# Optimization experiments

Hardware: AMD Instinct MI355X
Metric: run time of the kernel (lower is better)

Reference implementation:

```python
import jax, jax.numpy as jnp
import numpy as np

IN_FEATURES = 4096
OUT_FEATURES = 4096
GROUPS = 1
QB = 2 ** (8 - 1) - 1  # 127, int8 absmax quant


def setup_inputs() -> dict:
    key = jax.random.key(0)
    k_x, k_w = jax.random.split(key)
    x = jax.random.normal(k_x, (8192, IN_FEATURES), dtype=jnp.float32)
    # kaiming_uniform_(a=sqrt(5)) -> uniform(-1/sqrt(in), 1/sqrt(in))
    bound = 1.0 / np.sqrt(IN_FEATURES)
    weight = jax.random.uniform(
        k_w, (OUT_FEATURES, IN_FEATURES), dtype=jnp.float32,
        minval=-bound, maxval=bound)
    return {"input": x, "weight": weight}


def reference(input, weight):
    # --- ternarize weight per group ---
    w = weight.reshape(GROUPS, -1)                       # [G, out*in/G]
    w = w - jnp.mean(w, axis=1, keepdims=True)
    w = jnp.sign(w)
    # beta: per-group scale (note denominator uses full element count, as in source)
    beta = jnp.sum(jnp.abs(w), axis=1, keepdims=True) / (w.shape[0] * w.shape[1])
    w = (w * beta).reshape(OUT_FEATURES, IN_FEATURES)    # [out, in]

    # --- absmax int8 quantize activations (quantized values used, not dequant) ---
    scale = QB / jnp.max(jnp.abs(input))
    quant = jnp.round(scale * input)                     # [tokens, in]

    # --- linear + rescale ---
    out = quant @ w.T                                    # [tokens, out]
    out = out / beta.reshape(-1, 1)                      # groups=1: scalar divide
    return out
```

## Files before the change

kernel.cpp:

```cpp
#include <hip/hip_runtime.h>
#include <hip/hip_bf16.h>

typedef __attribute__((ext_vector_type(4))) int int4v;

#define TOKENS 8192
#define IN_F   4096
#define OUT_F  4096


__global__ void k_init(unsigned* maxbits) { *maxbits = 0u; }

__global__ __launch_bounds__(256) void k_wsum(const float4* __restrict__ w,
                                              double* __restrict__ partials) {
  __shared__ double sm[256];
  double s = 0.0;
  const float4* p = w + (size_t)blockIdx.x * 4096;
  for (int i = threadIdx.x; i < 4096; i += 256) {
    float4 v = p[i];
    s += (double)v.x + (double)v.y + (double)v.z + (double)v.w;
  }
  sm[threadIdx.x] = s;
  __syncthreads();
  for (int off = 128; off > 0; off >>= 1) {
    if (threadIdx.x < off) sm[threadIdx.x] += sm[threadIdx.x + off];
    __syncthreads();
  }
  if (threadIdx.x == 0) partials[blockIdx.x] = sm[0];
}

__global__ __launch_bounds__(256) void k_xmax(const float4* __restrict__ x,
                                              unsigned* __restrict__ maxbits) {
  float m = 0.f;
  const size_t n = (size_t)TOKENS * IN_F / 4;
  for (size_t i = (size_t)blockIdx.x * 256 + threadIdx.x; i < n;
       i += (size_t)gridDim.x * 256) {
    float4 v = x[i];
    m = fmaxf(m, fmaxf(fmaxf(fabsf(v.x), fabsf(v.y)),
                       fmaxf(fabsf(v.z), fabsf(v.w))));
  }
  __shared__ float sm[256];
  sm[threadIdx.x] = m;
  __syncthreads();
  for (int off = 128; off > 0; off >>= 1) {
    if (threadIdx.x < off) sm[threadIdx.x] = fmaxf(sm[threadIdx.x], sm[threadIdx.x + off]);
    __syncthreads();
  }
  if (threadIdx.x == 0) atomicMax(maxbits, __float_as_uint(sm[0]));
}

__global__ __launch_bounds__(256) void k_finalize(double* __restrict__ hdr,
                                                  const double* __restrict__ partials,
                                                  const unsigned* __restrict__ maxbits) {
  __shared__ double sm[256];
  double s = partials[threadIdx.x] + partials[threadIdx.x + 256] +
             partials[threadIdx.x + 512] + partials[threadIdx.x + 768];
  sm[threadIdx.x] = s;
  __syncthreads();
  for (int off = 128; off > 0; off >>= 1) {
    if (threadIdx.x < off) sm[threadIdx.x] += sm[threadIdx.x + off];
    __syncthreads();
  }
  if (threadIdx.x == 0) {
    hdr[0] = sm[0] / (double)((size_t)OUT_F * IN_F);
    hdr[1] = 127.0 / (double)__uint_as_float(*maxbits);
  }
}

__global__ __launch_bounds__(256) void k_quant(const float4* __restrict__ x,
                                               int* __restrict__ q,
                                               const double* __restrict__ hdr) {
  const double s = hdr[1];
  size_t i = (size_t)blockIdx.x * 256 + threadIdx.x;
  float4 v = x[i];
  int a = (int)rint(s * (double)v.x);
  int b = (int)rint(s * (double)v.y);
  int c = (int)rint(s * (double)v.z);
  int d = (int)rint(s * (double)v.w);
  q[i] = (a & 255) | ((b & 255) << 8) | ((c & 255) << 16) | ((d & 255) << 24);
}

__global__ __launch_bounds__(256) void k_tern(const float4* __restrict__ w,
                                              int* __restrict__ sgn,
                                              const double* __restrict__ hdr) {
  const double m = hdr[0];
  size_t i = (size_t)blockIdx.x * 256 + threadIdx.x;
  float4 v = w[i];
  int a = ((double)v.x > m) - ((double)v.x < m);
  int b = ((double)v.y > m) - ((double)v.y < m);
  int c = ((double)v.z > m) - ((double)v.z < m);
  int d = ((double)v.w > m) - ((double)v.w < m);
  sgn[i] = (a & 255) | ((b & 255) << 8) | ((c & 255) << 16) | ((d & 255) << 24);
}

__global__ __launch_bounds__(256) void k_gemm(const signed char* __restrict__ q,
                                              const signed char* __restrict__ s,
                                              float* __restrict__ out) {
  __shared__ signed char sA[128 * 128];
  __shared__ signed char sB[128 * 128];
  const int tid  = threadIdx.x;
  const int lane = tid & 63;
  const int wid  = tid >> 6;
  const int wr   = wid >> 1, wc = wid & 1;
  const int l15  = lane & 15, l4 = lane >> 4;
  const int bn = blockIdx.x & 31;
  const int bm = blockIdx.x >> 5;
  const size_t row0 = (size_t)bm * 128;
  const size_t col0 = (size_t)bn * 128;

  int4v acc[4][4];
#pragma unroll
  for (int i = 0; i < 4; ++i)
#pragma unroll
    for (int j = 0; j < 4; ++j) acc[i][j] = int4v{0, 0, 0, 0};

  for (int kt = 0; kt < 32; ++kt) {
    const int k0 = kt * 128;
    __syncthreads();
#pragma unroll
    for (int i = 0; i < 4; ++i) {
      const int idx_base = i * 256 + wid * 64;
      const int idx  = idx_base + lane;
      const int row  = idx >> 3;
      const int slot = idx & 7;
      const int koff = ((slot ^ (row & 7)) << 4);
      const signed char* gA = q + (row0 + row) * IN_F + k0 + koff;
      const signed char* gB = s + (col0 + row) * IN_F + k0 + koff;
      __builtin_amdgcn_global_load_lds(
          (const __attribute__((address_space(1))) void*)gA,
          (__attribute__((address_space(3))) void*)(sA + idx_base * 16), 16, 0, 0);
      __builtin_amdgcn_global_load_lds(
          (const __attribute__((address_space(1))) void*)gB,
          (__attribute__((address_space(3))) void*)(sB + idx_base * 16), 16, 0, 0);
    }
    __syncthreads();
#pragma unroll
    for (int ks = 0; ks < 2; ++ks) {
      int4v a[4], b[4];
#pragma unroll
      for (int f = 0; f < 4; ++f) {
        const int rowA = wr * 64 + f * 16 + l15;
        const int koff = ks * 64 + l4 * 16;
        a[f] = *(const int4v*)(sA + rowA * 128 + (koff ^ ((rowA & 7) << 4)));
        const int rowB = wc * 64 + f * 16 + l15;
        b[f] = *(const int4v*)(sB + rowB * 128 + (koff ^ ((rowB & 7) << 4)));
      }
#pragma unroll
      for (int fm = 0; fm < 4; ++fm)
#pragma unroll
        for (int fn = 0; fn < 4; ++fn)
          acc[fm][fn] = __builtin_amdgcn_mfma_i32_16x16x64_i8(a[fm], b[fn], acc[fm][fn], 0, 0, 0);
    }
  }

#pragma unroll
  for (int fm = 0; fm < 4; ++fm)
#pragma unroll
    for (int fn = 0; fn < 4; ++fn)
#pragma unroll
      for (int r = 0; r < 4; ++r) {
        const size_t rg = row0 + wr * 64 + fm * 16 + l4 * 4 + r;
        const size_t cg = col0 + wc * 64 + fn * 16 + l15;
        out[rg * OUT_F + cg] = (float)acc[fm][fn][r];
      }
}

extern "C" void kernel_launch(void* const* d_in, const int* in_sizes, int n_in,
                              void* d_out, int out_size, void* d_ws, size_t ws_size,
                              hipStream_t stream) {
  const float* x = (const float*)d_in[0];
  const float* w = (const float*)d_in[1];
  float* out = (float*)d_out;

  char* ws = (char*)d_ws;
  double*   hdr      = (double*)ws;
  unsigned* maxbits  = (unsigned*)(ws + 16);
  double*   partials = (double*)(ws + 1024);
  signed char* qbuf  = (signed char*)(ws + 16384);
  signed char* sbuf  = (signed char*)(ws + 16384 + (size_t)TOKENS * IN_F);

  k_init<<<1, 1, 0, stream>>>(maxbits);
  k_wsum<<<1024, 256, 0, stream>>>((const float4*)w, partials);
  k_xmax<<<2048, 256, 0, stream>>>((const float4*)x, maxbits);
  k_finalize<<<1, 256, 0, stream>>>(hdr, partials, maxbits);
  k_quant<<<(TOKENS * IN_F / 4) / 256, 256, 0, stream>>>((const float4*)x, (int*)qbuf, hdr);
  k_tern<<<(OUT_F * IN_F / 4) / 256, 256, 0, stream>>>((const float4*)w, (int*)sbuf, hdr);
  k_gemm<<<(TOKENS / 128) * (OUT_F / 128), 256, 0, stream>>>(qbuf, sbuf, out);
}
```

Baseline: 259.7 us.

## Rewrite int8 GEMM with 256x256 tiles and 4-stage async LDS pipeline

Replaces the 128x128 single-buffered GEMM with a 256x256 tile, 512-thread block that keeps a 4-deep ring of 64-wide K tiles in LDS. Global-to-LDS loads for future tiles are issued between interleaved MFMA halves, with explicit waitcnt, barriers and setprio to overlap memory with compute. It also swizzles the block index for L2 locality and changes the LDS XOR swizzle. The aim is to hide load latency and raise data reuse per block. The cost is a large accumulator register footprint and 128KB of LDS, which may limit occupancy, plus hand-placed synchronization that could be fragile.

Result: faster. 251.6 us (-3.1%).

```diff
diff --git a/kernel.cpp b/kernel.cpp
--- a/kernel.cpp
+++ b/kernel.cpp
@@ -92,75 +92,116 @@
   sgn[i] = (a & 255) | ((b & 255) << 8) | ((c & 255) << 16) | ((d & 255) << 24);
 }
 
-__global__ __launch_bounds__(256) void k_gemm(const signed char* __restrict__ q,
-                                              const signed char* __restrict__ s,
-                                              float* __restrict__ out) {
-  __shared__ signed char sA[128 * 128];
-  __shared__ signed char sB[128 * 128];
+__device__ __forceinline__ void stage2(const signed char* __restrict__ gsrc,
+                                       size_t grow0, int ktile,
+                                       signed char* ldsbase, int tid, int wid) {
+#pragma unroll
+  for (int i = 0; i < 2; ++i) {
+    const int slot = i * 512 + tid;
+    const int r = slot >> 2;
+    const int sir = slot & 3;
+    const signed char* g = gsrc + (grow0 + (size_t)r) * IN_F +
+                           (size_t)ktile * 64 + ((sir ^ (r & 3)) << 4);
+    __builtin_amdgcn_global_load_lds(
+        (const __attribute__((address_space(1))) void*)g,
+        (__attribute__((address_space(3))) void*)(ldsbase + (i * 512 + wid * 64) * 16),
+        16, 0, 0);
+  }
+}
+
+__global__ __launch_bounds__(512, 2) void k_gemm(const signed char* __restrict__ q,
+                                                 const signed char* __restrict__ s,
+                                                 float* __restrict__ out) {
+  __shared__ signed char sA[4][256 * 64];
+  __shared__ signed char sB[4][256 * 64];
   const int tid  = threadIdx.x;
   const int lane = tid & 63;
   const int wid  = tid >> 6;
-  const int wr   = wid >> 1, wc = wid & 1;
+  const int wm   = wid >> 2;
+  const int wn   = wid & 3;
   const int l15  = lane & 15, l4 = lane >> 4;
-  const int bn = blockIdx.x & 31;
-  const int bm = blockIdx.x >> 5;
-  const size_t row0 = (size_t)bm * 128;
-  const size_t col0 = (size_t)bn * 128;
-
-  int4v acc[4][4];
-#pragma unroll
-  for (int i = 0; i < 4; ++i)
+
+  const int swz = (blockIdx.x & 7) * 64 + (blockIdx.x >> 3);
+  const int bm = swz >> 4;
+  const int bn = swz & 15;
+  const size_t row0 = (size_t)bm * 256;
+  const size_t col0 = (size_t)bn * 256;
+
+  const int lane_off = l15 * 64 + ((l4 ^ (l15 & 3)) << 4);
+
+  int4v acc[8][4];
+#pragma unroll
+  for (int i = 0; i < 8; ++i)
 #pragma unroll
     for (int j = 0; j < 4; ++j) acc[i][j] = int4v{0, 0, 0, 0};
 
-  for (int kt = 0; kt < 32; ++kt) {
-    const int k0 = kt * 128;
-    __syncthreads();
-#pragma unroll
-    for (int i = 0; i < 4; ++i) {
-      const int idx_base = i * 256 + wid * 64;
-      const int idx  = idx_base + lane;
-      const int row  = idx >> 3;
-      const int slot = idx & 7;
-      const int koff = ((slot ^ (row & 7)) << 4);
-      const signed char* gA = q + (row0 + row) * IN_F + k0 + koff;
-      const signed char* gB = s + (col0 + row) * IN_F + k0 + koff;
-      __builtin_amdgcn_global_load_lds(
-          (const __attribute__((address_space(1))) void*)gA,
-          (__attribute__((address_space(3))) void*)(sA + idx_base * 16), 16, 0, 0);
-      __builtin_amdgcn_global_load_lds(
-          (const __attribute__((address_space(1))) void*)gB,
-          (__attribute__((address_space(3))) void*)(sB + idx_base * 16), 16, 0, 0);
+#pragma unroll
+  for (int t = 0; t < 3; ++t) {
+    stage2(q, row0, t, sA[t], tid, wid);
+    stage2(s, col0, t, sB[t], tid, wid);
+  }
+  asm volatile("s_waitcnt vmcnt(8)" ::: "memory");
+  __builtin_amdgcn_sched_barrier(0);
+  __builtin_amdgcn_s_barrier();
+  __builtin_amdgcn_sched_barrier(0);
+
+  for (int kt = 0; kt < 64; ++kt) {
+    const int c = kt & 3;
+    const int pf   = (kt + 3) & 63;
+    const int pbuf = (kt + 3) & 3;
+    const signed char* bufA = sA[c];
+    const signed char* bufB = sB[c];
+
+    int4v a[8], b0, b1;
+#pragma unroll
+    for (int m = 0; m < 8; ++m)
+      a[m] = *(const int4v*)(bufA + (wm * 128 + m * 16) * 64 + lane_off);
+    b0 = *(const int4v*)(bufB + (wn * 64 + 0) * 64 + lane_off);
+    b1 = *(const int4v*)(bufB + (wn * 64 + 16) * 64 + lane_off);
+    stage2(q, row0, pf, sA[pbuf], tid, wid);
+    __builtin_amdgcn_sched_barrier(0);
+    __builtin_amdgcn_s_barrier();
+    asm volatile("s_waitcnt lgkmcnt(0)" ::: "memory");
+    __builtin_amdgcn_sched_barrier(0);
+    __builtin_amdgcn_s_setprio(1);
+#pragma unroll
+    for (int m = 0; m < 8; ++m) {
+      acc[m][0] = __builtin_amdgcn_mfma_i32_16x16x64_i8(a[m], b0, acc[m][0], 0, 0, 0);
+      acc[m][1] = __builtin_amdgcn_mfma_i32_16x16x64_i8(a[m], b1, acc[m][1], 0, 0, 0);
     }
-    __syncthreads();
-#pragma unroll
-    for (int ks = 0; ks < 2; ++ks) {
-      int4v a[4], b[4];
-#pragma unroll
-      for (int f = 0; f < 4; ++f) {
-        const int rowA = wr * 64 + f * 16 + l15;
-        const int koff = ks * 64 + l4 * 16;
-        a[f] = *(const int4v*)(sA + rowA * 128 + (koff ^ ((rowA & 7) << 4)));
-        const int rowB = wc * 64 + f * 16 + l15;
-        b[f] = *(const int4v*)(sB + rowB * 128 + (koff ^ ((rowB & 7) << 4)));
-      }
-#pragma unroll
-      for (int fm = 0; fm < 4; ++fm)
-#pragma unroll
-        for (int fn = 0; fn < 4; ++fn)
-          acc[fm][fn] = __builtin_amdgcn_mfma_i32_16x16x64_i8(a[fm], b[fn], acc[fm][fn], 0, 0, 0);
+    __builtin_amdgcn_s_setprio(0);
+    __builtin_amdgcn_sched_barrier(0);
+    __builtin_amdgcn_s_barrier();
+
+    int4v b2 = *(const int4v*)(bufB + (wn * 64 + 32) * 64 + lane_off);
+    int4v b3 = *(const int4v*)(bufB + (wn * 64 + 48) * 64 + lane_off);
+    stage2(s, col0, pf, sB[pbuf], tid, wid);
+    __builtin_amdgcn_sched_barrier(0);
+    __builtin_amdgcn_s_barrier();
+    asm volatile("s_waitcnt lgkmcnt(0)" ::: "memory");
+    __builtin_amdgcn_sched_barrier(0);
+    __builtin_amdgcn_s_setprio(1);
+#pragma unroll
+    for (int m = 0; m < 8; ++m) {
+      acc[m][2] = __builtin_amdgcn_mfma_i32_16x16x64_i8(a[m], b2, acc[m][2], 0, 0, 0);
+      acc[m][3] = __builtin_amdgcn_mfma_i32_16x16x64_i8(a[m], b3, acc[m][3], 0, 0, 0);
     }
-  }
-
-#pragma unroll
-  for (int fm = 0; fm < 4; ++fm)
-#pragma unroll
-    for (int fn = 0; fn < 4; ++fn)
+    __builtin_amdgcn_s_setprio(0);
+    asm volatile("s_waitcnt vmcnt(8)" ::: "memory");
+    __builtin_amdgcn_sched_barrier(0);
+    __builtin_amdgcn_s_barrier();
+    __builtin_amdgcn_sched_barrier(0);
+  }
+
+#pragma unroll
+  for (int m = 0; m < 8; ++m)
+#pragma unroll
+    for (int n = 0; n < 4; ++n)
 #pragma unroll
       for (int r = 0; r < 4; ++r) {
-        const size_t rg = row0 + wr * 64 + fm * 16 + l4 * 4 + r;
-        const size_t cg = col0 + wc * 64 + fn * 16 + l15;
-        out[rg * OUT_F + cg] = (float)acc[fm][fn][r];
+        const size_t rg = row0 + wm * 128 + m * 16 + l4 * 4 + r;
+        const size_t cg = col0 + wn * 64 + n * 16 + l15;
+        out[rg * OUT_F + cg] = (float)acc[m][n][r];
       }
 }
 
@@ -184,5 +225,5 @@
   k_finalize<<<1, 256, 0, stream>>>(hdr, partials, maxbits);
   k_quant<<<(TOKENS * IN_F / 4) / 256, 256, 0, stream>>>((const float4*)x, (int*)qbuf, hdr);
   k_tern<<<(OUT_F * IN_F / 4) / 256, 256, 0, stream>>>((const float4*)w, (int*)sbuf, hdr);
-  k_gemm<<<(TOKENS / 128) * (OUT_F / 128), 256, 0, stream>>>(qbuf, sbuf, out);
-}
+  k_gemm<<<(TOKENS / 256) * (OUT_F / 256), 512, 0, stream>>>(qbuf, sbuf, out);
+}
```
